# Kernel tuning notes

Measured on AMD Instinct MI355X. Metric: run time of the kernel, lower is better.

## Reference

```python
import jax, jax.numpy as jnp
import numpy as np

GROUP_SIZE = 8
REQUIRED_ZEROS = 4


def _dorefa_quantize(x, bits):
    # tanh-normalize-round
    t = jnp.tanh(x).astype(jnp.float32)
    y = t / jnp.max(jnp.abs(t))
    delta = float(2 ** (bits - 1) - 1)
    _y = jnp.round(y * delta)

    out_c, in_c, h, w = _y.shape
    if in_c < GROUP_SIZE:
        return _y / delta

    g = in_c // GROUP_SIZE
    keep = GROUP_SIZE - REQUIRED_ZEROS  # keep at most 4 non-zeros per group

    # [out_c, g*8, h, w] -> [out_c, g, h, w, 8] (group axis last for top_k)
    yg = _y[:, : g * GROUP_SIZE].reshape(out_c, g, GROUP_SIZE, h, w)
    yg = jnp.transpose(yg, (0, 1, 3, 4, 2))

    # The torch loop zeroes the smallest-|v| non-zeros until >=4 zeros per
    # group. Equivalently: keep only the `keep` largest-|v| entries of each
    # group (zeros have |v|=0, so groups already having >=4 zeros are
    # unchanged). Fully vectorized via batched top-k + one-hot mask.
    absv = jnp.abs(yg)
    _, idx = jax.lax.top_k(absv, keep)                      # [o,g,h,w,keep]
    mask = jax.nn.one_hot(idx, GROUP_SIZE, dtype=yg.dtype).sum(axis=-2)
    yg = yg * mask                                          # [o,g,h,w,8]

    yg = jnp.transpose(yg, (0, 1, 4, 2, 3)).reshape(out_c, g * GROUP_SIZE, h, w)
    out = jnp.concatenate([yg, _y[:, g * GROUP_SIZE :]], axis=1) if g * GROUP_SIZE < in_c else yg
    return out / delta


def setup_inputs() -> dict:
    key = jax.random.key(0)
    x = jax.random.normal(key, (2048, 2048, 3, 3), dtype=jnp.float32)
    return {"x": x, "bits": 8}


def reference(x, bits):
    return _dorefa_quantize(x, bits)
```

## Files before the change

kernel.cpp:

```cpp
#include <hip/hip_runtime.h>
#include <math.h>

#define HW        9
#define GROUP     8
#define KEEP      4
#define DELTA     127.0f
#define INV_DELTA (1.0f / 127.0f)

__global__ void maxabs_kernel(const float4* __restrict__ x, unsigned* __restrict__ ws, int n4) {
    __shared__ float red[4];
    float m = 0.0f;
    int stride = gridDim.x * blockDim.x;
    for (int i = blockIdx.x * blockDim.x + threadIdx.x; i < n4; i += stride) {
        float4 v = x[i];
        m = fmaxf(m, fmaxf(fmaxf(fabsf(v.x), fabsf(v.y)),
                           fmaxf(fabsf(v.z), fabsf(v.w))));
    }
    #pragma unroll
    for (int off = 32; off > 0; off >>= 1)
        m = fmaxf(m, __shfl_down(m, off, 64));
    int wave = threadIdx.x >> 6;
    if ((threadIdx.x & 63) == 0) red[wave] = m;
    __syncthreads();
    if (threadIdx.x == 0) {
        float b = fmaxf(fmaxf(red[0], red[1]), fmaxf(red[2], red[3]));
        atomicMax(ws, __float_as_uint(b));
    }
}

__device__ __forceinline__ float fast_tanh(float x) {
    float ax  = fabsf(x);
    float axc = fminf(ax, 10.0f);
    float E   = __expf(2.0f * axc);
    float num = E - 1.0f;
    float den = E + 1.0f;
    float r0  = __builtin_amdgcn_rcpf(den);
    float r   = r0 * fmaf(-den, r0, 2.0f);
    float tl  = copysignf(num * r, x);
    float s = x * x;
    float p = fmaf(s, 0.021869489f, -0.05396825f);
    p = fmaf(s, p, 0.13333334f);
    p = fmaf(s, p, -0.33333334f);
    float ts = fmaf(x * s, p, x);
    return (ax <= 0.25f) ? ts : tl;
}

__global__ void quant_kernel(const float* __restrict__ x,
                             float* __restrict__ out,
                             const unsigned* __restrict__ ws,
                             int n_cells, int cells_per_o) {
    __shared__ float sM, sC;
    if (threadIdx.x == 0) {
        float mm = (float)tanh((double)__uint_as_float(*ws));
        sM = mm;
        sC = (float)(127.0 / (double)mm);
    }
    __syncthreads();
    float M = sM, C = sC;

    int cell = blockIdx.x * blockDim.x + threadIdx.x;
    if (cell >= n_cells) return;

    int o  = cell / cells_per_o;
    int r  = cell - o * cells_per_o;
    int g  = r / HW;
    int hw = r - g * HW;

    size_t base = (size_t)o * (size_t)cells_per_o * GROUP + (size_t)g * (GROUP * HW) + hw;
    const float* p = x + base;
    float*       q = out + base;

    float v[GROUP];
    float a[GROUP];
    #pragma unroll
    for (int j = 0; j < GROUP; ++j) {
        float xx = p[j * HW];
        float t  = fast_tanh(xx);
        float z  = t * C;
        float rz = rintf(z);
        float d  = 0.5f - fabsf(z - rz);
        if (d < 6e-6f * fabsf(z) + 3e-6f) {
            float td = (float)tanh((double)xx);
            float y  = td / M;
            z  = y * DELTA;
            rz = rintf(z);
        }
        v[j] = rz;
        a[j] = fabsf(rz);
    }

    #pragma unroll
    for (int j = 0; j < GROUP; ++j) {
        int cnt = 0;
        #pragma unroll
        for (int i = 0; i < GROUP; ++i) {
            cnt += (a[i] > a[j]) || (a[i] == a[j] && i < j);
        }
        q[j * HW] = (cnt < KEEP) ? (v[j] * INV_DELTA) : 0.0f;
    }
}

extern "C" void kernel_launch(void* const* d_in, const int* in_sizes, int n_in,
                              void* d_out, int out_size, void* d_ws, size_t ws_size,
                              hipStream_t stream) {
    const float* x = (const float*)d_in[0];
    float* out = (float*)d_out;
    unsigned* ws = (unsigned*)d_ws;

    int n = in_sizes[0];
    int n4 = n / 4;
    int n_cells = n / GROUP;
    int cells_per_o = 256 * HW;

    hipMemsetAsync(ws, 0, sizeof(unsigned), stream);

    maxabs_kernel<<<2048, 256, 0, stream>>>((const float4*)x, ws, n4);

    int blocks = (n_cells + 255) / 256;
    quant_kernel<<<blocks, 256, 0, stream>>>(x, out, ws, n_cells, cells_per_o);
}
```

Measured before the change: 318.2 us.

## Process whole 72-float channel groups per thread with float4 loads and pairwise ranking

Each thread now owns one contiguous 8x9 group block and loads and stores it with float4 accesses, replacing strided scalar loads at stride 9. Ranking within a group uses pairwise comparisons instead of counting for each element. The tanh polynomial is extended so the cheap path covers up to |x|<=0.5, the rare double-precision fallback is moved into a noinline helper with a tighter tie threshold, and the maxabs loop is unrolled. The 72-float register array per thread raises register pressure and lowers occupancy, and each thread's contiguous 288-byte access pattern leaves loads across the wave poorly coalesced.

After: 308.3 us. 3.1% less time.

```diff
diff --git a/kernel.cpp b/kernel.cpp
--- a/kernel.cpp
+++ b/kernel.cpp
@@ -6,11 +6,13 @@
 #define KEEP      4
 #define DELTA     127.0f
 #define INV_DELTA (1.0f / 127.0f)
+#define GB_FLOATS 72
 
 __global__ void maxabs_kernel(const float4* __restrict__ x, unsigned* __restrict__ ws, int n4) {
     __shared__ float red[4];
     float m = 0.0f;
     int stride = gridDim.x * blockDim.x;
+    #pragma unroll 4
     for (int i = blockIdx.x * blockDim.x + threadIdx.x; i < n4; i += stride) {
         float4 v = x[i];
         m = fmaxf(m, fmaxf(fmaxf(fabsf(v.x), fabsf(v.y)),
@@ -28,6 +30,12 @@
     }
 }
 
+__device__ __attribute__((noinline)) float ref_rz(float xx, float M) {
+    float td = (float)tanh((double)xx);
+    float y  = td / M;
+    return rintf(y * DELTA);
+}
+
 __device__ __forceinline__ float fast_tanh(float x) {
     float ax  = fabsf(x);
     float axc = fminf(ax, 10.0f);
@@ -38,17 +46,19 @@
     float r   = r0 * fmaf(-den, r0, 2.0f);
     float tl  = copysignf(num * r, x);
     float s = x * x;
-    float p = fmaf(s, 0.021869489f, -0.05396825f);
+    float p = fmaf(s, 0.0035921280f, -0.0088632358f);
+    p = fmaf(s, p, 0.021869488f);
+    p = fmaf(s, p, -0.053968254f);
     p = fmaf(s, p, 0.13333334f);
     p = fmaf(s, p, -0.33333334f);
     float ts = fmaf(x * s, p, x);
-    return (ax <= 0.25f) ? ts : tl;
+    return (ax <= 0.5f) ? ts : tl;
 }
 
-__global__ void quant_kernel(const float* __restrict__ x,
-                             float* __restrict__ out,
+__global__ void quant_kernel(const float4* __restrict__ x,
+                             float4* __restrict__ out,
                              const unsigned* __restrict__ ws,
-                             int n_cells, int cells_per_o) {
+                             int n_gb) {
     __shared__ float sM, sC;
     if (threadIdx.x == 0) {
         float mm = (float)tanh((double)__uint_as_float(*ws));
@@ -58,45 +68,57 @@
     __syncthreads();
     float M = sM, C = sC;
 
-    int cell = blockIdx.x * blockDim.x + threadIdx.x;
-    if (cell >= n_cells) return;
+    int gb = blockIdx.x * blockDim.x + threadIdx.x;
+    if (gb >= n_gb) return;
 
-    int o  = cell / cells_per_o;
-    int r  = cell - o * cells_per_o;
-    int g  = r / HW;
-    int hw = r - g * HW;
+    const float4* p = x   + (size_t)gb * (GB_FLOATS / 4);
+    float4*       q = out + (size_t)gb * (GB_FLOATS / 4);
 
-    size_t base = (size_t)o * (size_t)cells_per_o * GROUP + (size_t)g * (GROUP * HW) + hw;
-    const float* p = x + base;
-    float*       q = out + base;
-
-    float v[GROUP];
-    float a[GROUP];
+    float f[GB_FLOATS];
     #pragma unroll
-    for (int j = 0; j < GROUP; ++j) {
-        float xx = p[j * HW];
-        float t  = fast_tanh(xx);
-        float z  = t * C;
-        float rz = rintf(z);
-        float d  = 0.5f - fabsf(z - rz);
-        if (d < 6e-6f * fabsf(z) + 3e-6f) {
-            float td = (float)tanh((double)xx);
-            float y  = td / M;
-            z  = y * DELTA;
-            rz = rintf(z);
-        }
-        v[j] = rz;
-        a[j] = fabsf(rz);
+    for (int k = 0; k < GB_FLOATS / 4; ++k) {
+        float4 v = p[k];
+        f[4 * k + 0] = v.x; f[4 * k + 1] = v.y;
+        f[4 * k + 2] = v.z; f[4 * k + 3] = v.w;
     }
 
     #pragma unroll
-    for (int j = 0; j < GROUP; ++j) {
-        int cnt = 0;
+    for (int hw = 0; hw < HW; ++hw) {
+        float v8[GROUP], a8[GROUP];
+        #pragma unroll
+        for (int j = 0; j < GROUP; ++j) {
+            float xx = f[j * HW + hw];
+            float t  = fast_tanh(xx);
+            float z  = t * C;
+            float rz = rintf(z);
+            float d  = 0.5f - fabsf(z - rz);
+            if (d < fmaf(2e-6f, fabsf(z), 5e-7f))
+                rz = ref_rz(xx, M);
+            v8[j] = rz;
+            a8[j] = fabsf(rz);
+        }
+        int rank[GROUP] = {0, 0, 0, 0, 0, 0, 0, 0};
         #pragma unroll
         for (int i = 0; i < GROUP; ++i) {
-            cnt += (a[i] > a[j]) || (a[i] == a[j] && i < j);
+            #pragma unroll
+            for (int j = i + 1; j < GROUP; ++j) {
+                bool ge = (a8[i] >= a8[j]);
+                rank[j] += ge ? 1 : 0;
+                rank[i] += ge ? 0 : 1;
+            }
         }
-        q[j * HW] = (cnt < KEEP) ? (v[j] * INV_DELTA) : 0.0f;
+        #pragma unroll
+        for (int j = 0; j < GROUP; ++j) {
+            f[j * HW + hw] = (rank[j] < KEEP) ? (v8[j] * INV_DELTA) : 0.0f;
+        }
+    }
+
+    #pragma unroll
+    for (int k = 0; k < GB_FLOATS / 4; ++k) {
+        float4 v;
+        v.x = f[4 * k + 0]; v.y = f[4 * k + 1];
+        v.z = f[4 * k + 2]; v.w = f[4 * k + 3];
+        q[k] = v;
     }
 }
 
@@ -109,13 +131,12 @@
 
     int n = in_sizes[0];
     int n4 = n / 4;
-    int n_cells = n / GROUP;
-    int cells_per_o = 256 * HW;
+    int n_gb = n / GB_FLOATS;
 
     hipMemsetAsync(ws, 0, sizeof(unsigned), stream);
 
     maxabs_kernel<<<2048, 256, 0, stream>>>((const float4*)x, ws, n4);
 
-    int blocks = (n_cells + 255) / 256;
-    quant_kernel<<<blocks, 256, 0, stream>>>(x, out, ws, n_cells, cells_per_o);
+    int blocks = (n_gb + 255) / 256;
+    quant_kernel<<<blocks, 256, 0, stream>>>((const float4*)x, (float4*)out, ws, n_gb);
 }
```
